# Kernel optimization log

Measured on AMD Instinct MI355X. Metric: run time of the kernel, lower is better.

The kernel has to match this reference:

```python
import jax, jax.numpy as jnp
import numpy as np
import math

B, N, EPG = 128, 512, 8192            # graphs, nodes/graph, edges/graph
E = B * EPG
DIN, H, DOUT = 128, 128, 10
RATIO = 0.8
K1 = math.ceil(RATIO * N)             # 410 nodes/graph after pool 1
K2 = math.ceil(RATIO * K1)            # 328 nodes/graph after pool 2
EPS = 1e-5


def setup_inputs() -> dict:
    key = jax.random.key(0)
    ks = jax.random.split(key, 16)
    x = jax.random.normal(ks[0], (B * N, DIN), jnp.float32)
    gid = jnp.repeat(jnp.arange(B, dtype=jnp.int32), EPG)
    src = jax.random.randint(ks[1], (E,), 0, N, dtype=jnp.int32) + gid * N
    dst = jax.random.randint(ks[2], (E,), 0, N, dtype=jnp.int32) + gid * N
    edge_index = jnp.stack([src, dst])

    def w(k, shape, fan_in):
        return jax.random.uniform(k, shape, jnp.float32, -1.0, 1.0) / np.sqrt(fan_in).astype(np.float32)

    return {
        "x": x, "edge_index": edge_index,
        "conv1_W": w(ks[3], (DIN, H), DIN), "conv1_b": jnp.zeros((H,), jnp.float32),
        "conv2_W": w(ks[4], (H, H), H),     "conv2_b": jnp.zeros((H,), jnp.float32),
        "score1_W": w(ks[5], (H, 1), H),    "score1_b": jnp.zeros((1,), jnp.float32),
        "score2_W": w(ks[6], (H, 1), H),    "score2_b": jnp.zeros((1,), jnp.float32),
        "bn1_g": jnp.ones((H,), jnp.float32), "bn1_b": jnp.zeros((H,), jnp.float32),
        "bn1_m": 0.1 * jax.random.normal(ks[7], (H,), jnp.float32),
        "bn1_v": jax.random.uniform(ks[8], (H,), jnp.float32, 0.5, 1.5),
        "bn2_g": jnp.ones((H,), jnp.float32), "bn2_b": jnp.zeros((H,), jnp.float32),
        "bn2_m": 0.1 * jax.random.normal(ks[9], (H,), jnp.float32),
        "bn2_v": jax.random.uniform(ks[10], (H,), jnp.float32, 0.5, 1.5),
        "lin0_W": w(ks[11], (DOUT, DIN), DIN), "lin0_b": jnp.zeros((DOUT,), jnp.float32),
        "lin1_W": w(ks[12], (DOUT, H), H),     "lin1_b": jnp.zeros((DOUT,), jnp.float32),
        "lin2_W": w(ks[13], (DOUT, H), H),     "lin2_b": jnp.zeros((DOUT,), jnp.float32),
    }


def gcn(h_in, src, dst, emask, W, b, n):
    # PyG GCNConv: self-loops + symmetric normalization D^-1/2 (A+I) D^-1/2 (XW) + b
    deg = jnp.ones((n,), h_in.dtype).at[dst].add(emask)      # self-loop counts as 1
    dinv = jax.lax.rsqrt(deg)
    coef = (dinv[src] * dinv[dst] * emask)[:, None]          # masked-out edges -> 0
    h = h_in @ W
    agg = jnp.zeros_like(h).at[dst].add(h[src] * coef)
    return agg + h * (dinv * dinv)[:, None] + b              # self-loop message + bias


def sag_pool(x, score, src, dst, emask, n_per, k):
    # topk per graph (equal-sized graphs -> static shapes), x <- x[perm]*tanh(score[perm])
    idx = jax.lax.top_k(score.reshape(B, n_per), k)[1]                      # [B,k]
    perm = (idx.astype(jnp.int32) + (jnp.arange(B, dtype=jnp.int32) * n_per)[:, None]).reshape(-1)
    xn = x[perm] * jnp.tanh(score[perm])[:, None]
    # filter_adj: remap surviving nodes, mask edges touching dropped nodes
    remap = jnp.full((B * n_per,), -1, jnp.int32).at[perm].set(jnp.arange(B * k, dtype=jnp.int32))
    s2, d2 = remap[src], remap[dst]
    em2 = emask * (s2 >= 0).astype(emask.dtype) * (d2 >= 0).astype(emask.dtype)
    return xn, jnp.maximum(s2, 0), jnp.maximum(d2, 0), em2


def bn_relu(x, g, b, m, v):
    # eval-mode BatchNorm1d followed by ReLU
    return jax.nn.relu(g * (x - m) * jax.lax.rsqrt(v + EPS) + b)


def reference(x, edge_index, conv1_W, conv1_b, conv2_W, conv2_b,
              score1_W, score1_b, score2_W, score2_b,
              bn1_g, bn1_b, bn1_m, bn1_v, bn2_g, bn2_b, bn2_m, bn2_v,
              lin0_W, lin0_b, lin1_W, lin1_b, lin2_W, lin2_b):
    src, dst = edge_index[0], edge_index[1]
    emask = jnp.ones((E,), x.dtype)
    hidden = [(x, N)]
    # layer 0: GCNConv -> SAGPool -> BN -> ReLU
    h = gcn(x, src, dst, emask, conv1_W, conv1_b, B * N)
    s = gcn(h, src, dst, emask, score1_W, score1_b, B * N)[:, 0]
    h, src, dst, emask = sag_pool(h, s, src, dst, emask, N, K1)
    h = bn_relu(h, bn1_g, bn1_b, bn1_m, bn1_v)
    hidden.append((h, K1))
    # layer 1
    h = gcn(h, src, dst, emask, conv2_W, conv2_b, B * K1)
    s = gcn(h, src, dst, emask, score2_W, score2_b, B * K1)[:, 0]
    h, src, dst, emask = sag_pool(h, s, src, dst, emask, K1, K2)
    h = bn_relu(h, bn2_g, bn2_b, bn2_m, bn2_v)
    hidden.append((h, K2))
    # jumping-knowledge readout: global_add_pool each rep, per-layer linear, sum (dropout eval = id)
    lins = [(lin0_W, lin0_b), (lin1_W, lin1_b), (lin2_W, lin2_b)]
    out = jnp.zeros((B, DOUT), x.dtype)
    for (hh, n_per), (W, bb) in zip(hidden, lins):
        pooled = hh.reshape(B, n_per, -1).sum(axis=1)   # global_add_pool (segment sum)
        out = out + pooled @ W.T + bb
    return out
```

## Files before the change

kernel.cpp:

```cpp
#include <hip/hip_runtime.h>

#define Bg   128
#define NPG  512
#define EPGc 8192
#define Etot (Bg*EPGc)
#define DOUTc 10
#define K1c  410
#define K2c  328
#define N0c  (Bg*NPG)
#define N1c  (Bg*K1c)
#define N2c  (Bg*K2c)
#define EPSc 1e-5f

typedef __attribute__((ext_vector_type(8))) short s8v;
typedef __attribute__((ext_vector_type(4))) float f4v;

static __device__ __forceinline__ unsigned short bf_rne(float x) {
  unsigned u = __float_as_uint(x);
  u += 0x7FFFu + ((u >> 16) & 1u);
  return (unsigned short)(u >> 16);
}
static __device__ __forceinline__ float bf_f(unsigned short h) {
  return __uint_as_float(((unsigned)h) << 16);
}

static __global__ __launch_bounds__(512) void k_prep0(const int* __restrict__ src,
                                                      const int* __restrict__ dst,
                                                      const float* __restrict__ W1,
                                                      const float* __restrict__ W2,
                                                      unsigned short* __restrict__ pk,
                                                      float* __restrict__ dinv,
                                                      int* __restrict__ rp,
                                                      int2* __restrict__ e2,
                                                      float* __restrict__ pooled) {
  __shared__ int    cnt[NPG];
  __shared__ float  sdv[NPG];
  __shared__ int    srp[NPG];
  __shared__ int    sbuf[512];
  int g = blockIdx.x, tid = threadIdx.x;
  cnt[tid] = 0;
  if (tid < 128) {
    pooled[g * 128 + tid] = 0.f;
    pooled[Bg * 128 + g * 128 + tid] = 0.f;
    pooled[2 * Bg * 128 + g * 128 + tid] = 0.f;
  }
  if (tid < 256) {
    int i = g * 256 + tid;
    const float* W = (i < 16384) ? W1 : W2;
    unsigned short* d = pk + ((i < 16384) ? 0 : 32768);
    int ii = i & 16383;
    int grp = ii >> 9, lane = (ii >> 3) & 63, j = ii & 7;
    int kk = grp >> 3, t = grp & 7;
    int k = kk * 32 + (lane >> 4) * 8 + j;
    int n = t * 16 + (lane & 15);
    float w = W[k * 128 + n];
    unsigned short hi = bf_rne(w);
    d[ii] = hi;
    d[16384 + ii] = bf_rne(w - bf_f(hi));
  }
  __syncthreads();
  const int* sp = src + (size_t)g * EPGc;
  const int* dp = dst + (size_t)g * EPGc;
  for (int e = tid; e < EPGc; e += 512) atomicAdd(&cnt[dp[e] - g * NPG], 1);
  __syncthreads();
  int c = cnt[tid];
  float dv = 1.0f / sqrtf(1.0f + (float)c);
  sdv[tid] = dv;
  dinv[g * NPG + tid] = dv;
  sbuf[tid] = c;
  __syncthreads();
  for (int off = 1; off < 512; off <<= 1) {
    int t = (tid >= off) ? sbuf[tid - off] : 0;
    __syncthreads();
    sbuf[tid] += t;
    __syncthreads();
  }
  srp[tid] = sbuf[tid] - c;
  rp[g * (NPG + 1) + tid] = sbuf[tid] - c;
  if (tid == 511) rp[g * (NPG + 1) + NPG] = sbuf[511];
  cnt[tid] = 0;
  __syncthreads();
  for (int e = tid; e < EPGc; e += 512) {
    int s = sp[e], d = dp[e];
    int dl = d - g * NPG;
    int pos = srp[dl] + atomicAdd(&cnt[dl], 1);
    e2[(size_t)g * EPGc + pos] =
        make_int2(s, __float_as_int(sdv[s - g * NPG] * sdv[dl]));
  }
}

static __global__ __launch_bounds__(128) void k_xsum(const float* __restrict__ x,
                                                     float* __restrict__ pooled0) {
  int g = blockIdx.x >> 4, c = blockIdx.x & 15;
  int f = threadIdx.x;
  float acc = 0.f;
  const float* p = x + ((size_t)g * NPG + c * 32) * 128 + f;
  for (int i = 0; i < 32; ++i, p += 128) acc += *p;
  atomicAdd(&pooled0[g * 128 + f], acc);
}

static __global__ __launch_bounds__(256) void k_gemm3(const float* __restrict__ X,
                                                      const unsigned short* __restrict__ pk,
                                                      float* __restrict__ Y) {
  __shared__ unsigned short wl[32768];
  int tid = threadIdx.x;
  for (int i = tid; i < 4096; i += 256) ((int4*)wl)[i] = ((const int4*)pk)[i];
  int wv = tid >> 6, lane = tid & 63;
  int q = lane >> 4, m16 = lane & 15;
  size_t row = (size_t)blockIdx.x * 64 + wv * 16 + m16;
  s8v ahi[4], alo[4];
#pragma unroll
  for (int kk = 0; kk < 4; ++kk) {
    const float* xr = X + row * 128 + kk * 32 + q * 8;
    float4 a0 = *(const float4*)xr;
    float4 a1 = *(const float4*)(xr + 4);
    float av[8] = {a0.x, a0.y, a0.z, a0.w, a1.x, a1.y, a1.z, a1.w};
    union { unsigned short u[8]; s8v v; } H, L;
#pragma unroll
    for (int j = 0; j < 8; ++j) {
      unsigned short h = bf_rne(av[j]);
      H.u[j] = h;
      L.u[j] = bf_rne(av[j] - bf_f(h));
    }
    ahi[kk] = H.v; alo[kk] = L.v;
  }
  __syncthreads();
  int orow0 = blockIdx.x * 64 + wv * 16 + q * 4;
#pragma unroll
  for (int t = 0; t < 8; ++t) {
    f4v acc = {0.f, 0.f, 0.f, 0.f};
#pragma unroll
    for (int kk = 0; kk < 4; ++kk) {
      s8v bhi = *(const s8v*)&wl[(kk * 8 + t) * 512 + lane * 8];
      s8v blo = *(const s8v*)&wl[16384 + (kk * 8 + t) * 512 + lane * 8];
      acc = __builtin_amdgcn_mfma_f32_16x16x32_bf16(ahi[kk], bhi, acc, 0, 0, 0);
      acc = __builtin_amdgcn_mfma_f32_16x16x32_bf16(alo[kk], bhi, acc, 0, 0, 0);
      acc = __builtin_amdgcn_mfma_f32_16x16x32_bf16(ahi[kk], blo, acc, 0, 0, 0);
    }
#pragma unroll
    for (int r = 0; r < 4; ++r)
      Y[(size_t)(orow0 + r) * 128 + t * 16 + m16] = acc[r];
  }
}

template <int NPER, int RG>
static __global__ __launch_bounds__(256) void k_agg3(const float* __restrict__ h0,
                                                     const float* __restrict__ dinv,
                                                     const float* __restrict__ bias,
                                                     const int* __restrict__ rp,
                                                     const int2* __restrict__ e2,
                                                     const float* __restrict__ sw,
                                                     float* __restrict__ h1,
                                                     float* __restrict__ spre) {
  int tid = threadIdx.x;
  int hw = tid >> 5, l = tid & 31;
  int b = blockIdx.x;
  int xcd = b & 7, slot = b >> 3;
  int g = xcd * 16 + (slot & 15);
  int rowgrp = slot >> 4;
  int li = rowgrp * 8 + hw;
  if (li >= NPER) return;
  int j = g * NPER + li;
  const int* rpg = rp + g * (NPER + 1);
  int start = rpg[li], end = rpg[li + 1];
  const int2* ep = e2 + (size_t)g * EPGc;
  float di = dinv[j];
  float sc = di * di;
  float4 acc = *(const float4*)&h0[(size_t)j * 128 + l * 4];
  float4 bb = ((const float4*)bias)[l];
  acc.x = acc.x * sc + bb.x; acc.y = acc.y * sc + bb.y;
  acc.z = acc.z * sc + bb.z; acc.w = acc.w * sc + bb.w;
  int e = start;
  for (; e + 4 <= end; e += 4) {
    int2 p0 = ep[e], p1 = ep[e + 1], p2 = ep[e + 2], p3 = ep[e + 3];
    float4 v0 = *(const float4*)&h0[(size_t)p0.x * 128 + l * 4];
    float4 v1 = *(const float4*)&h0[(size_t)p1.x * 128 + l * 4];
    float4 v2 = *(const float4*)&h0[(size_t)p2.x * 128 + l * 4];
    float4 v3 = *(const float4*)&h0[(size_t)p3.x * 128 + l * 4];
    float c0 = __int_as_float(p0.y), c1 = __int_as_float(p1.y);
    float c2 = __int_as_float(p2.y), c3 = __int_as_float(p3.y);
    acc.x += v0.x * c0 + v1.x * c1 + v2.x * c2 + v3.x * c3;
    acc.y += v0.y * c0 + v1.y * c1 + v2.y * c2 + v3.y * c3;
    acc.z += v0.z * c0 + v1.z * c1 + v2.z * c2 + v3.z * c3;
    acc.w += v0.w * c0 + v1.w * c1 + v2.w * c2 + v3.w * c3;
  }
  for (; e < end; ++e) {
    int2 pp = ep[e];
    float c = __int_as_float(pp.y);
    float4 v = *(const float4*)&h0[(size_t)pp.x * 128 + l * 4];
    acc.x += v.x * c; acc.y += v.y * c; acc.z += v.z * c; acc.w += v.w * c;
  }
  ((float4*)&h1[(size_t)j * 128])[l] = acc;
  float4 w4 = ((const float4*)sw)[l];
  float pr = acc.x * w4.x + acc.y * w4.y + acc.z * w4.z + acc.w * w4.w;
#pragma unroll
  for (int off = 16; off; off >>= 1) pr += __shfl_xor(pr, off, 64);
  if (l == 0) spre[j] = pr;
}

template <int NPER>
static __global__ void k_score2(const float* __restrict__ spre, const float* __restrict__ dinv,
                                const float* __restrict__ bptr, const int* __restrict__ rp,
                                const int2* __restrict__ e2, float* __restrict__ s, int n) {
  int j = blockIdx.x * 256 + threadIdx.x;
  if (j >= n) return;
  int g = j / NPER, li = j - g * NPER;
  const int* rpg = rp + g * (NPER + 1);
  int start = rpg[li], end = rpg[li + 1];
  const int2* ep = e2 + (size_t)g * EPGc;
  float di = dinv[j];
  float acc = spre[j] * di * di + bptr[0];
  int e = start;
  for (; e + 8 <= end; e += 8) {
    int2 p[8];
#pragma unroll
    for (int q = 0; q < 8; ++q) p[q] = ep[e + q];
    float a[8];
#pragma unroll
    for (int q = 0; q < 8; ++q) a[q] = spre[p[q].x];
#pragma unroll
    for (int q = 0; q < 8; ++q) acc += a[q] * __int_as_float(p[q].y);
  }
  for (; e + 4 <= end; e += 4) {
    int2 p0 = ep[e], p1 = ep[e + 1], p2 = ep[e + 2], p3 = ep[e + 3];
    float a0 = spre[p0.x], a1 = spre[p1.x], a2 = spre[p2.x], a3 = spre[p3.x];
    acc += a0 * __int_as_float(p0.y) + a1 * __int_as_float(p1.y) +
           a2 * __int_as_float(p2.y) + a3 * __int_as_float(p3.y);
  }
  for (; e < end; ++e) { int2 pp = ep[e]; acc += spre[pp.x] * __int_as_float(pp.y); }
  s[j] = acc;
}

template <int NPER, int K>
static __global__ __launch_bounds__(512) void k_repool(const float* __restrict__ sv,
                                                       const int* __restrict__ src,
                                                       const int* __restrict__ dst,
                                                       int* __restrict__ perm,
                                                       float* __restrict__ dinv2,
                                                       int* __restrict__ rp2,
                                                       int2* __restrict__ e2) {
  __shared__ float sc[512];
  __shared__ int   sidx[512];
  __shared__ short rmp[NPER];
  __shared__ int   cnt[K];
  __shared__ float sdv[K];
  __shared__ int   srp[K];
  __shared__ int   sbuf[512];
  int g = blockIdx.x, tid = threadIdx.x;
  sc[tid] = (tid < NPER) ? sv[g * NPER + tid] : -3.402823466e38f;
  sidx[tid] = tid;
  if (tid < NPER) rmp[tid] = -1;
  __syncthreads();
  for (int kk = 2; kk <= 512; kk <<= 1) {
    for (int j = kk >> 1; j > 0; j >>= 1) {
      int i = tid, p = i ^ j;
      if (p > i) {
        bool up = ((i & kk) == 0);
        float si = sc[i], sp2 = sc[p];
        if (up ? (si < sp2) : (si > sp2)) {
          sc[i] = sp2; sc[p] = si;
          int t = sidx[i]; sidx[i] = sidx[p]; sidx[p] = t;
        }
      }
      __syncthreads();
    }
  }
  if (tid < K) {
    perm[g * K + tid] = g * NPER + sidx[tid];
    rmp[sidx[tid]] = (short)tid;
    cnt[tid] = 0;
  }
  __syncthreads();
  const int* sp = src + (size_t)g * EPGc;
  const int* dp = dst + (size_t)g * EPGc;
  for (int e = tid; e < EPGc; e += 512) {
    int s = rmp[sp[e] - g * NPER];
    int d = rmp[dp[e] - g * NPER];
    if ((s | d) >= 0) atomicAdd(&cnt[d], 1);
  }
  __syncthreads();
  int c = (tid < K) ? cnt[tid] : 0;
  if (tid < K) {
    float dv = 1.0f / sqrtf(1.0f + (float)c);
    sdv[tid] = dv;
    dinv2[g * K + tid] = dv;
  }
  sbuf[tid] = c;
  __syncthreads();
  for (int off = 1; off < 512; off <<= 1) {
    int t = (tid >= off) ? sbuf[tid - off] : 0;
    __syncthreads();
    sbuf[tid] += t;
    __syncthreads();
  }
  if (tid < K) { srp[tid] = sbuf[tid] - c; rp2[g * (K + 1) + tid] = sbuf[tid] - c; cnt[tid] = 0; }
  if (tid == 511) rp2[g * (K + 1) + K] = sbuf[511];
  __syncthreads();
  for (int e = tid; e < EPGc; e += 512) {
    int s = rmp[sp[e] - g * NPER];
    int d = rmp[dp[e] - g * NPER];
    if ((s | d) >= 0) {
      int pos = srp[d] + atomicAdd(&cnt[d], 1);
      e2[(size_t)g * EPGc + pos] = make_int2(g * K + s, __float_as_int(sdv[s] * sdv[d]));
    }
  }
}

template <int NPER, int K>
static __global__ __launch_bounds__(256) void k_topk(const float* __restrict__ s,
                                                     int* __restrict__ perm) {
  __shared__ float sc[512];
  __shared__ int   idx[512];
  int g = blockIdx.x, tid = threadIdx.x;
  for (int i = tid; i < 512; i += 256) {
    if (i < NPER) { sc[i] = s[g * NPER + i]; idx[i] = i; }
    else          { sc[i] = -3.402823466e38f; idx[i] = 0; }
  }
  __syncthreads();
  for (int kk = 2; kk <= 512; kk <<= 1) {
    for (int j = kk >> 1; j > 0; j >>= 1) {
      for (int base = 0; base < 512; base += 256) {
        int i = base + tid;
        int p = i ^ j;
        if (p > i) {
          bool up = ((i & kk) == 0);
          float si = sc[i], sp = sc[p];
          if (up ? (si < sp) : (si > sp)) {
            sc[i] = sp; sc[p] = si;
            int t = idx[i]; idx[i] = idx[p]; idx[p] = t;
          }
        }
      }
      __syncthreads();
    }
  }
  for (int r = tid; r < K; r += 256) perm[g * K + r] = g * NPER + idx[r];
}

template <int NPER, int CH, bool WXP>
static __global__ __launch_bounds__(128) void k_poolbn(const float* __restrict__ h,
                                                       const float* __restrict__ s,
                                                       const int* __restrict__ perm,
                                                       const float* __restrict__ gg,
                                                       const float* __restrict__ bb,
                                                       const float* __restrict__ mm,
                                                       const float* __restrict__ vv,
                                                       float* __restrict__ xp,
                                                       float* __restrict__ pooledseg) {
  int g = blockIdx.x / CH, cidx = blockIdx.x - g * CH;
  int f = threadIdx.x;
  const int rows = (NPER + CH - 1) / CH;
  int r0 = cidx * rows, r1 = min(NPER, r0 + rows);
  if (r0 >= r1) return;
  float G = gg[f], Bb = bb[f], Mm = mm[f];
  float inv = 1.0f / sqrtf(vv[f] + EPSc);
  float acc = 0.f;
  for (int r = r0; r < r1; ++r) {
    int j = g * NPER + r;
    int old = perm[j];
    float t = tanhf(s[old]);
    float val = h[(size_t)old * 128 + f] * t;
    float o = fmaxf(G * (val - Mm) * inv + Bb, 0.f);
    if (WXP) xp[(size_t)j * 128 + f] = o;
    acc += o;
  }
  atomicAdd(&pooledseg[g * 128 + f], acc);
}

static __global__ void k_final(const float* __restrict__ pooled,
                               const float* __restrict__ w0, const float* __restrict__ b0,
                               const float* __restrict__ w1, const float* __restrict__ b1,
                               const float* __restrict__ w2, const float* __restrict__ b2,
                               float* __restrict__ out) {
  int t = blockIdx.x * 256 + threadIdx.x;
  if (t >= Bg * DOUTc) return;
  int g = t / DOUTc, o = t - g * DOUTc;
  const float* p0 = pooled + g * 128;
  const float* p1 = pooled + Bg * 128 + g * 128;
  const float* p2 = pooled + 2 * Bg * 128 + g * 128;
  float acc = b0[o] + b1[o] + b2[o];
  for (int k = 0; k < 128; ++k)
    acc += p0[k] * w0[o * 128 + k] + p1[k] * w1[o * 128 + k] + p2[k] * w2[o * 128 + k];
  out[t] = acc;
}

extern "C" void kernel_launch(void* const* d_in, const int* in_sizes, int n_in,
                              void* d_out, int out_size, void* d_ws, size_t ws_size,
                              hipStream_t stream) {
  (void)in_sizes; (void)n_in; (void)out_size; (void)ws_size;
  const float* x    = (const float*)d_in[0];
  const int*   ei   = (const int*)d_in[1];
  const int*   src0 = ei;
  const int*   dst0 = ei + Etot;
  const float* c1W = (const float*)d_in[2];  const float* c1b = (const float*)d_in[3];
  const float* c2W = (const float*)d_in[4];  const float* c2b = (const float*)d_in[5];
  const float* s1W = (const float*)d_in[6];  const float* s1b = (const float*)d_in[7];
  const float* s2W = (const float*)d_in[8];  const float* s2b = (const float*)d_in[9];
  const float* bn1g = (const float*)d_in[10]; const float* bn1b = (const float*)d_in[11];
  const float* bn1m = (const float*)d_in[12]; const float* bn1v = (const float*)d_in[13];
  const float* bn2g = (const float*)d_in[14]; const float* bn2b = (const float*)d_in[15];
  const float* bn2m = (const float*)d_in[16]; const float* bn2v = (const float*)d_in[17];
  const float* l0W = (const float*)d_in[18]; const float* l0b = (const float*)d_in[19];
  const float* l1W = (const float*)d_in[20]; const float* l1b = (const float*)d_in[21];
  const float* l2W = (const float*)d_in[22]; const float* l2b = (const float*)d_in[23];
  float* out = (float*)d_out;

  char* p = (char*)d_ws;
  auto alloc = [&](size_t bytes) { char* q = p; p += (bytes + 255) & ~(size_t)255; return q; };
  float* h0    = (float*)alloc((size_t)N0c * 128 * 4);
  float* h1    = (float*)alloc((size_t)N0c * 128 * 4);
  float* xp1   = (float*)alloc((size_t)N1c * 128 * 4);
  float* dinv  = (float*)alloc((size_t)N0c * 4);
  float* dinv2 = (float*)alloc((size_t)N1c * 4);
  int*   rp    = (int*)alloc((size_t)Bg * (NPG + 1) * 4);
  int*   rp2   = (int*)alloc((size_t)Bg * (K1c + 1) * 4);
  int2*  e2    = (int2*)alloc((size_t)Etot * 8);
  float* spre  = (float*)alloc((size_t)N0c * 4);
  float* sv    = (float*)alloc((size_t)N0c * 4);
  int*   perm  = (int*)alloc((size_t)N1c * 4);
  unsigned short* pk = (unsigned short*)alloc((size_t)65536 * 2);
  float* pooled= (float*)alloc((size_t)3 * Bg * 128 * 4);

  dim3 b256(256), b512(512), b128(128);

  k_prep0<<<Bg, b512, 0, stream>>>(src0, dst0, c1W, c2W, pk, dinv, rp, e2, pooled);
  k_xsum<<<Bg * 16, b128, 0, stream>>>(x, pooled);
  k_gemm3<<<N0c / 64, b256, 0, stream>>>(x, pk, h0);
  k_agg3<NPG, 64><<<128 * 64, b256, 0, stream>>>(h0, dinv, c1b, rp, e2, s1W, h1, spre);
  k_score2<NPG><<<(N0c + 255) / 256, b256, 0, stream>>>(spre, dinv, s1b, rp, e2, sv, N0c);
  k_repool<NPG, K1c><<<Bg, b512, 0, stream>>>(sv, src0, dst0, perm, dinv2, rp2, e2);
  k_poolbn<K1c, 16, true><<<Bg * 16, b128, 0, stream>>>(h1, sv, perm, bn1g, bn1b, bn1m, bn1v,
                                                        xp1, pooled + Bg * 128);

  float* g1 = h0;
  float* h2 = h1;
  k_gemm3<<<N1c / 64, b256, 0, stream>>>(xp1, pk + 32768, g1);
  k_agg3<K1c, 52><<<128 * 52, b256, 0, stream>>>(g1, dinv2, c2b, rp2, e2, s2W, h2, spre);
  k_score2<K1c><<<(N1c + 255) / 256, b256, 0, stream>>>(spre, dinv2, s2b, rp2, e2, sv, N1c);
  k_topk<K1c, K2c><<<Bg, b256, 0, stream>>>(sv, perm);
  k_poolbn<K2c, 16, false><<<Bg * 16, b128, 0, stream>>>(h2, sv, perm, bn2g, bn2b, bn2m, bn2v,
                                                         nullptr, pooled + 2 * Bg * 128);

  k_final<<<(Bg * DOUTc + 255) / 256, b256, 0, stream>>>(pooled, l0W, l0b, l1W, l1b, l2W, l2b, out);
}
```

Before: 339.7 us.

## Fuse score aggregation into top-k kernels and global pool into first GEMM

Removes the separate k_xsum and k_score2 launches. The layer-0 input sum is folded into the first GEMM using wavefront shuffles and atomics, and the score aggregation is computed per graph from shared memory inside the repool and top-k kernels. The tanh of the selected scores is precomputed once and stored per selected node, so the pool/BN kernel no longer gathers scores and recomputes tanh for every feature. This cuts launch overhead and global traffic, but score aggregation now runs on only 128 blocks, one per graph, with serial per-node loops, and the GEMM takes on extra shuffles and atomics.

```diff
diff --git a/kernel.cpp b/kernel.cpp
--- a/kernel.cpp
+++ b/kernel.cpp
@@ -89,25 +89,17 @@
   }
 }
 
-static __global__ __launch_bounds__(128) void k_xsum(const float* __restrict__ x,
-                                                     float* __restrict__ pooled0) {
-  int g = blockIdx.x >> 4, c = blockIdx.x & 15;
-  int f = threadIdx.x;
-  float acc = 0.f;
-  const float* p = x + ((size_t)g * NPG + c * 32) * 128 + f;
-  for (int i = 0; i < 32; ++i, p += 128) acc += *p;
-  atomicAdd(&pooled0[g * 128 + f], acc);
-}
-
 static __global__ __launch_bounds__(256) void k_gemm3(const float* __restrict__ X,
                                                       const unsigned short* __restrict__ pk,
-                                                      float* __restrict__ Y) {
+                                                      float* __restrict__ Y,
+                                                      float* __restrict__ p0) {
   __shared__ unsigned short wl[32768];
   int tid = threadIdx.x;
   for (int i = tid; i < 4096; i += 256) ((int4*)wl)[i] = ((const int4*)pk)[i];
   int wv = tid >> 6, lane = tid & 63;
   int q = lane >> 4, m16 = lane & 15;
   size_t row = (size_t)blockIdx.x * 64 + wv * 16 + m16;
+  float* pg = p0 ? (p0 + (size_t)(blockIdx.x >> 3) * 128) : nullptr;
   s8v ahi[4], alo[4];
 #pragma unroll
   for (int kk = 0; kk < 4; ++kk) {
@@ -115,6 +107,15 @@
     float4 a0 = *(const float4*)xr;
     float4 a1 = *(const float4*)(xr + 4);
     float av[8] = {a0.x, a0.y, a0.z, a0.w, a1.x, a1.y, a1.z, a1.w};
+    if (pg) {
+#pragma unroll
+      for (int j = 0; j < 8; ++j) {
+        float v = av[j];
+        v += __shfl_xor(v, 1, 64); v += __shfl_xor(v, 2, 64);
+        v += __shfl_xor(v, 4, 64); v += __shfl_xor(v, 8, 64);
+        if (m16 == 0) atomicAdd(&pg[kk * 32 + q * 8 + j], v);
+      }
+    }
     union { unsigned short u[8]; s8v v; } H, L;
 #pragma unroll
     for (int j = 0; j < 8; ++j) {
@@ -198,47 +199,19 @@
   if (l == 0) spre[j] = pr;
 }
 
-template <int NPER>
-static __global__ void k_score2(const float* __restrict__ spre, const float* __restrict__ dinv,
-                                const float* __restrict__ bptr, const int* __restrict__ rp,
-                                const int2* __restrict__ e2, float* __restrict__ s, int n) {
-  int j = blockIdx.x * 256 + threadIdx.x;
-  if (j >= n) return;
-  int g = j / NPER, li = j - g * NPER;
-  const int* rpg = rp + g * (NPER + 1);
-  int start = rpg[li], end = rpg[li + 1];
-  const int2* ep = e2 + (size_t)g * EPGc;
-  float di = dinv[j];
-  float acc = spre[j] * di * di + bptr[0];
-  int e = start;
-  for (; e + 8 <= end; e += 8) {
-    int2 p[8];
-#pragma unroll
-    for (int q = 0; q < 8; ++q) p[q] = ep[e + q];
-    float a[8];
-#pragma unroll
-    for (int q = 0; q < 8; ++q) a[q] = spre[p[q].x];
-#pragma unroll
-    for (int q = 0; q < 8; ++q) acc += a[q] * __int_as_float(p[q].y);
-  }
-  for (; e + 4 <= end; e += 4) {
-    int2 p0 = ep[e], p1 = ep[e + 1], p2 = ep[e + 2], p3 = ep[e + 3];
-    float a0 = spre[p0.x], a1 = spre[p1.x], a2 = spre[p2.x], a3 = spre[p3.x];
-    acc += a0 * __int_as_float(p0.y) + a1 * __int_as_float(p1.y) +
-           a2 * __int_as_float(p2.y) + a3 * __int_as_float(p3.y);
-  }
-  for (; e < end; ++e) { int2 pp = ep[e]; acc += spre[pp.x] * __int_as_float(pp.y); }
-  s[j] = acc;
-}
-
 template <int NPER, int K>
-static __global__ __launch_bounds__(512) void k_repool(const float* __restrict__ sv,
+static __global__ __launch_bounds__(512) void k_repool(const float* __restrict__ spre,
+                                                       const float* __restrict__ dinv,
+                                                       const float* __restrict__ sb,
+                                                       const int* __restrict__ rp,
                                                        const int* __restrict__ src,
                                                        const int* __restrict__ dst,
                                                        int* __restrict__ perm,
+                                                       float* __restrict__ tsel,
                                                        float* __restrict__ dinv2,
                                                        int* __restrict__ rp2,
                                                        int2* __restrict__ e2) {
+  __shared__ float ss[NPER];
   __shared__ float sc[512];
   __shared__ int   sidx[512];
   __shared__ short rmp[NPER];
@@ -247,9 +220,28 @@
   __shared__ int   srp[K];
   __shared__ int   sbuf[512];
   int g = blockIdx.x, tid = threadIdx.x;
-  sc[tid] = (tid < NPER) ? sv[g * NPER + tid] : -3.402823466e38f;
+  if (tid < NPER) { ss[tid] = spre[g * NPER + tid]; rmp[tid] = -1; }
+  __syncthreads();
+  if (tid < NPER) {
+    const int* rpg = rp + g * (NPER + 1);
+    int st = rpg[tid], en = rpg[tid + 1];
+    const int2* ep = e2 + (size_t)g * EPGc;
+    float di = dinv[g * NPER + tid];
+    float acc = ss[tid] * di * di + sb[0];
+    int e = st;
+    for (; e + 4 <= en; e += 4) {
+      int2 p0 = ep[e], p1 = ep[e + 1], p2 = ep[e + 2], p3 = ep[e + 3];
+      acc += ss[p0.x - g * NPER] * __int_as_float(p0.y) +
+             ss[p1.x - g * NPER] * __int_as_float(p1.y) +
+             ss[p2.x - g * NPER] * __int_as_float(p2.y) +
+             ss[p3.x - g * NPER] * __int_as_float(p3.y);
+    }
+    for (; e < en; ++e) { int2 pp = ep[e]; acc += ss[pp.x - g * NPER] * __int_as_float(pp.y); }
+    sc[tid] = acc;
+  } else {
+    sc[tid] = -3.402823466e38f;
+  }
   sidx[tid] = tid;
-  if (tid < NPER) rmp[tid] = -1;
   __syncthreads();
   for (int kk = 2; kk <= 512; kk <<= 1) {
     for (int j = kk >> 1; j > 0; j >>= 1) {
@@ -267,6 +259,7 @@
   }
   if (tid < K) {
     perm[g * K + tid] = g * NPER + sidx[tid];
+    tsel[g * K + tid] = tanhf(sc[tid]);
     rmp[sidx[tid]] = (short)tid;
     cnt[tid] = 0;
   }
@@ -307,39 +300,63 @@
 }
 
 template <int NPER, int K>
-static __global__ __launch_bounds__(256) void k_topk(const float* __restrict__ s,
-                                                     int* __restrict__ perm) {
+static __global__ __launch_bounds__(512) void k_topk2(const float* __restrict__ spre,
+                                                      const float* __restrict__ dinv2,
+                                                      const float* __restrict__ sb,
+                                                      const int* __restrict__ rp2,
+                                                      const int2* __restrict__ e2,
+                                                      int* __restrict__ perm,
+                                                      float* __restrict__ tsel) {
+  __shared__ float ss[NPER];
   __shared__ float sc[512];
-  __shared__ int   idx[512];
+  __shared__ int   sidx[512];
   int g = blockIdx.x, tid = threadIdx.x;
-  for (int i = tid; i < 512; i += 256) {
-    if (i < NPER) { sc[i] = s[g * NPER + i]; idx[i] = i; }
-    else          { sc[i] = -3.402823466e38f; idx[i] = 0; }
-  }
+  if (tid < NPER) ss[tid] = spre[g * NPER + tid];
+  __syncthreads();
+  if (tid < NPER) {
+    const int* rpg = rp2 + g * (NPER + 1);
+    int st = rpg[tid], en = rpg[tid + 1];
+    const int2* ep = e2 + (size_t)g * EPGc;
+    float di = dinv2[g * NPER + tid];
+    float acc = ss[tid] * di * di + sb[0];
+    int e = st;
+    for (; e + 4 <= en; e += 4) {
+      int2 p0 = ep[e], p1 = ep[e + 1], p2 = ep[e + 2], p3 = ep[e + 3];
+      acc += ss[p0.x - g * NPER] * __int_as_float(p0.y) +
+             ss[p1.x - g * NPER] * __int_as_float(p1.y) +
+             ss[p2.x - g * NPER] * __int_as_float(p2.y) +
+             ss[p3.x - g * NPER] * __int_as_float(p3.y);
+    }
+    for (; e < en; ++e) { int2 pp = ep[e]; acc += ss[pp.x - g * NPER] * __int_as_float(pp.y); }
+    sc[tid] = acc;
+  } else {
+    sc[tid] = -3.402823466e38f;
+  }
+  sidx[tid] = tid;
   __syncthreads();
   for (int kk = 2; kk <= 512; kk <<= 1) {
     for (int j = kk >> 1; j > 0; j >>= 1) {
-      for (int base = 0; base < 512; base += 256) {
-        int i = base + tid;
-        int p = i ^ j;
-        if (p > i) {
-          bool up = ((i & kk) == 0);
-          float si = sc[i], sp = sc[p];
-          if (up ? (si < sp) : (si > sp)) {
-            sc[i] = sp; sc[p] = si;
-            int t = idx[i]; idx[i] = idx[p]; idx[p] = t;
-          }
+      int i = tid, p = i ^ j;
+      if (p > i) {
+        bool up = ((i & kk) == 0);
+        float si = sc[i], sp2 = sc[p];
+        if (up ? (si < sp2) : (si > sp2)) {
+          sc[i] = sp2; sc[p] = si;
+          int t = sidx[i]; sidx[i] = sidx[p]; sidx[p] = t;
         }
       }
       __syncthreads();
     }
   }
-  for (int r = tid; r < K; r += 256) perm[g * K + r] = g * NPER + idx[r];
+  if (tid < K) {
+    perm[g * K + tid] = g * NPER + sidx[tid];
+    tsel[g * K + tid] = tanhf(sc[tid]);
+  }
 }
 
 template <int NPER, int CH, bool WXP>
 static __global__ __launch_bounds__(128) void k_poolbn(const float* __restrict__ h,
-                                                       const float* __restrict__ s,
+                                                       const float* __restrict__ tsel,
                                                        const int* __restrict__ perm,
                                                        const float* __restrict__ gg,
                                                        const float* __restrict__ bb,
@@ -358,8 +375,7 @@
   for (int r = r0; r < r1; ++r) {
     int j = g * NPER + r;
     int old = perm[j];
-    float t = tanhf(s[old]);
-    float val = h[(size_t)old * 128 + f] * t;
+    float val = h[(size_t)old * 128 + f] * tsel[j];
     float o = fmaxf(G * (val - Mm) * inv + Bb, 0.f);
     if (WXP) xp[(size_t)j * 128 + f] = o;
     acc += o;
@@ -416,7 +432,7 @@
   int*   rp2   = (int*)alloc((size_t)Bg * (K1c + 1) * 4);
   int2*  e2    = (int2*)alloc((size_t)Etot * 8);
   float* spre  = (float*)alloc((size_t)N0c * 4);
-  float* sv    = (float*)alloc((size_t)N0c * 4);
+  float* tsel  = (float*)alloc((size_t)N1c * 4);
   int*   perm  = (int*)alloc((size_t)N1c * 4);
   unsigned short* pk = (unsigned short*)alloc((size_t)65536 * 2);
   float* pooled= (float*)alloc((size_t)3 * Bg * 128 * 4);
@@ -424,22 +440,21 @@
   dim3 b256(256), b512(512), b128(128);
 
   k_prep0<<<Bg, b512, 0, stream>>>(src0, dst0, c1W, c2W, pk, dinv, rp, e2, pooled);
-  k_xsum<<<Bg * 16, b128, 0, stream>>>(x, pooled);
-  k_gemm3<<<N0c / 64, b256, 0, stream>>>(x, pk, h0);
+  k_gemm3<<<N0c / 64, b256, 0, stream>>>(x, pk, h0, pooled);
   k_agg3<NPG, 64><<<128 * 64, b256, 0, stream>>>(h0, dinv, c1b, rp, e2, s1W, h1, spre);
-  k_score2<NPG><<<(N0c + 255) / 256, b256, 0, stream>>>(spre, dinv, s1b, rp, e2, sv, N0c);
-  k_repool<NPG, K1c><<<Bg, b512, 0, stream>>>(sv, src0, dst0, perm, dinv2, rp2, e2);
-  k_poolbn<K1c, 16, true><<<Bg * 16, b128, 0, stream>>>(h1, sv, perm, bn1g, bn1b, bn1m, bn1v,
-                                                        xp1, pooled + Bg * 128);
+  k_repool<NPG, K1c><<<Bg, b512, 0, stream>>>(spre, dinv, s1b, rp, src0, dst0,
+                                              perm, tsel, dinv2, rp2, e2);
+  k_poolbn<K1c, 16, true><<<Bg * 16, b128, 0, stream>>>(h1, tsel, perm, bn1g, bn1b,
+                                                        bn1m, bn1v, xp1, pooled + Bg * 128);
 
   float* g1 = h0;
   float* h2 = h1;
-  k_gemm3<<<N1c / 64, b256, 0, stream>>>(xp1, pk + 32768, g1);
+  k_gemm3<<<N1c / 64, b256, 0, stream>>>(xp1, pk + 32768, g1, nullptr);
   k_agg3<K1c, 52><<<128 * 52, b256, 0, stream>>>(g1, dinv2, c2b, rp2, e2, s2W, h2, spre);
-  k_score2<K1c><<<(N1c + 255) / 256, b256, 0, stream>>>(spre, dinv2, s2b, rp2, e2, sv, N1c);
-  k_topk<K1c, K2c><<<Bg, b256, 0, stream>>>(sv, perm);
-  k_poolbn<K2c, 16, false><<<Bg * 16, b128, 0, stream>>>(h2, sv, perm, bn2g, bn2b, bn2m, bn2v,
-                                                         nullptr, pooled + 2 * Bg * 128);
+  k_topk2<K1c, K2c><<<Bg, b512, 0, stream>>>(spre, dinv2, s2b, rp2, e2, perm, tsel);
+  k_poolbn<K2c, 16, false><<<Bg * 16, b128, 0, stream>>>(h2, tsel, perm, bn2g, bn2b,
+                                                         bn2m, bn2v, nullptr,
+                                                         pooled + 2 * Bg * 128);
 
   k_final<<<(Bg * DOUTc + 255) / 256, b256, 0, stream>>>(pooled, l0W, l0b, l1W, l1b, l2W, l2b, out);
 }
```

New measurement: 334.8 us. Within noise of the previous version (-1.4%).
